# Performance work log

Hardware: AMD Instinct MI355X
Metric: run time of the kernel (lower is better)

Reference implementation:

```python
import jax, jax.numpy as jnp
import numpy as np

H = 8192  # hidden_size == input_size
NNZ = 1_000_000
B = 128
T = 64


def _spmm(rows, cols, values, x, out_dim):
    # y[r, :] += v * x[c, :] for each nnz (r, c, v); matches coalesced COO spmm
    gathered = values[:, None] * x[cols]          # [nnz, B]
    return jax.ops.segment_sum(gathered, rows, num_segments=out_dim)  # [out_dim, B]


def setup_inputs() -> dict:
    key = jax.random.key(0)
    ks = jax.random.split(key, 5)
    x = jax.random.normal(ks[0], (B, T, H), dtype=jnp.float32)
    ih_indices = jax.random.randint(ks[1], (2, NNZ), 0, H, dtype=jnp.int32)
    hh_indices = jax.random.randint(ks[2], (2, NNZ), 0, H, dtype=jnp.int32)
    # scale so tanh pre-activations stay in a reasonable range (~122 nnz/row)
    ih_values = jax.random.normal(ks[3], (NNZ,), dtype=jnp.float32) * 0.05
    hh_values = jax.random.normal(ks[4], (NNZ,), dtype=jnp.float32) * 0.05
    bias_ih = jnp.zeros((H, 1), dtype=jnp.float32)
    bias_hh = jnp.zeros((H, 1), dtype=jnp.float32)
    return {
        "x": x,
        "ih_indices": ih_indices,
        "ih_values": ih_values,
        "hh_indices": hh_indices,
        "hh_values": hh_values,
        "bias_ih": bias_ih,
        "bias_hh": bias_hh,
    }


def reference(x, ih_indices, ih_values, hh_indices, hh_values, bias_ih, bias_hh):
    # x: (batch, seq, features) -> (T, F, B) as in torch permute(1, 2, 0)
    xs = jnp.transpose(x, (1, 2, 0))  # [T, H, B]
    ih_r, ih_c = ih_indices[0], ih_indices[1]
    hh_r, hh_c = hh_indices[0], hh_indices[1]

    def step(h, x_t):
        pre = (_spmm(ih_r, ih_c, ih_values, x_t, H) + bias_ih
               + _spmm(hh_r, hh_c, hh_values, h, H) + bias_hh)
        h_new = jnp.tanh(pre)
        return h_new, h_new

    h0 = jnp.zeros((H, x.shape[0]), dtype=x.dtype)
    _, out = jax.lax.scan(step, h0, xs)  # out: [T, H, B]
    return jnp.transpose(out, (2, 0, 1))  # [B, T, H] (batch_first)
```

## Files before the change

kernel.cpp:

```cpp
#include <hip/hip_runtime.h>
#include <cstdint>
#include <cstddef>
#include <cstring>

#define H 8192
#define NNZ 1000000
#define B 128
#define T 64

typedef unsigned int u32;
typedef u32 u32x2 __attribute__((ext_vector_type(2)));

__device__ inline float bf_lo(u32 w) { return __uint_as_float(w << 16); }
__device__ inline float bf_hi(u32 w) { return __uint_as_float(w & 0xffff0000u); }
__device__ inline unsigned short f2bf(float f) {
    u32 v = __float_as_uint(f);
    v += 0x7fffu + ((v >> 16) & 1u);
    return (unsigned short)(v >> 16);
}
__device__ inline u32 pack_bf16(float a, float b) {
    return (u32)f2bf(a) | ((u32)f2bf(b) << 16);
}
__device__ inline float fast_tanh(float x) {
    float e = __expf(2.0f * x);
    return 1.0f - 2.0f / (e + 1.0f);
}

__device__ inline void spmm_row(const int* __restrict__ rp, const int2* __restrict__ pair,
                                const char* __restrict__ basep, int r, bool hi, u32 i8,
                                float& ax, float& ay, float& az, float& aw) {
    int s = rp[r], e = rp[r + 1];
    int j = s;
    for (; j + 16 <= e; j += 16) {
        int2 q[16];
        #pragma unroll
        for (int u = 0; u < 16; ++u) q[u] = pair[j + u];
        u32x2 g[8];
        #pragma unroll
        for (int u = 0; u < 8; ++u) {
            u32 c = (u32)(hi ? q[2 * u + 1].x : q[2 * u].x);
            g[u] = *(const u32x2*)(basep + ((c << 8) + i8));
        }
        #pragma unroll
        for (int u = 0; u < 8; ++u) {
            float v = __int_as_float(hi ? q[2 * u + 1].y : q[2 * u].y);
            ax = fmaf(v, bf_lo(g[u].x), ax);
            ay = fmaf(v, bf_hi(g[u].x), ay);
            az = fmaf(v, bf_lo(g[u].y), az);
            aw = fmaf(v, bf_hi(g[u].y), aw);
        }
    }
    for (; j + 2 <= e; j += 2) {
        int2 q0 = pair[j], q1 = pair[j + 1];
        u32 c = (u32)(hi ? q1.x : q0.x);
        u32x2 g = *(const u32x2*)(basep + ((c << 8) + i8));
        float v = __int_as_float(hi ? q1.y : q0.y);
        ax = fmaf(v, bf_lo(g.x), ax);
        ay = fmaf(v, bf_hi(g.x), ay);
        az = fmaf(v, bf_lo(g.y), az);
        aw = fmaf(v, bf_hi(g.y), aw);
    }
    if (j < e) {
        int2 q0 = pair[j];
        u32 c = (u32)q0.x;
        u32x2 g = *(const u32x2*)(basep + ((c << 8) + i8));
        float v = hi ? 0.0f : __int_as_float(q0.y);
        ax = fmaf(v, bf_lo(g.x), ax);
        ay = fmaf(v, bf_hi(g.x), ay);
        az = fmaf(v, bf_lo(g.y), az);
        aw = fmaf(v, bf_hi(g.y), aw);
    }
}

__global__ void hist2_kernel(const int* __restrict__ rows_a, const int* __restrict__ rows_b,
                             int* __restrict__ cnt_a, int* __restrict__ cnt_b) {
    int j = blockIdx.x * blockDim.x + threadIdx.x;
    if (j < NNZ) atomicAdd(&cnt_a[rows_a[j]], 1);
    else if (j < 2 * NNZ) atomicAdd(&cnt_b[rows_b[j - NNZ]], 1);
}

__global__ void scan_kernel(const int* __restrict__ cnt0, int* __restrict__ rp0, int* __restrict__ cur0,
                            const int* __restrict__ cnt1, int* __restrict__ rp1, int* __restrict__ cur1) {
    const int* cnt = (blockIdx.x == 0) ? cnt0 : cnt1;
    int* rp  = (blockIdx.x == 0) ? rp0 : rp1;
    int* cur = (blockIdx.x == 0) ? cur0 : cur1;
    __shared__ int buf[1024];
    __shared__ int carry;
    int tid = threadIdx.x;
    if (tid == 0) carry = 0;
    __syncthreads();
    for (int base = 0; base < H; base += 1024) {
        int v = cnt[base + tid];
        buf[tid] = v;
        __syncthreads();
        for (int off = 1; off < 1024; off <<= 1) {
            int t = (tid >= off) ? buf[tid - off] : 0;
            __syncthreads();
            buf[tid] += t;
            __syncthreads();
        }
        int incl = buf[tid];
        int excl = incl - v;
        int c = carry;
        rp[base + tid]  = c + excl;
        cur[base + tid] = c + excl;
        __syncthreads();
        if (tid == 1023) carry = c + incl;
        __syncthreads();
    }
    if (tid == 0) rp[H] = carry;
}

__global__ void scatter2_kernel(const int* __restrict__ ra, const int* __restrict__ ca,
                                const float* __restrict__ va, int* __restrict__ cur_a,
                                int2* __restrict__ pa,
                                const int* __restrict__ rb, const int* __restrict__ cb,
                                const float* __restrict__ vb, int* __restrict__ cur_b,
                                int2* __restrict__ pb) {
    int j = blockIdx.x * blockDim.x + threadIdx.x;
    if (j < NNZ) {
        int r = ra[j];
        int p = atomicAdd(&cur_a[r], 1);
        pa[p] = make_int2(ca[j], __float_as_int(va[j]));
    } else if (j < 2 * NNZ) {
        int jj = j - NNZ;
        int r = rb[jj];
        int p = atomicAdd(&cur_b[r], 1);
        pb[p] = make_int2(cb[jj], __float_as_int(vb[jj]));
    }
}

__global__ void transpose_bf16_kernel(const float* __restrict__ src, u32* __restrict__ dst) {
    __shared__ float tile[32][33];
    int c0 = blockIdx.x * 32;
    int r0 = blockIdx.y * 32;
    int x = threadIdx.x, y = threadIdx.y;
    #pragma unroll
    for (int i = y; i < 32; i += 8) {
        tile[i][x] = src[(size_t)(r0 + i) * (T * H) + (c0 + x)];
    }
    __syncthreads();
    int tid = y * 32 + x;
    #pragma unroll
    for (int idx = tid; idx < 32 * 16; idx += 256) {
        int row = idx >> 4, w = idx & 15;
        u32 word = pack_bf16(tile[2 * w][row], tile[2 * w + 1][row]);
        dst[(size_t)(c0 + row) * 64 + (r0 >> 1) + w] = word;
    }
}

__global__ void transpose_out_kernel(const u32* __restrict__ src, float* __restrict__ dst) {
    __shared__ u32 tile[32][33];
    int c0 = blockIdx.x * 32;
    int w0 = blockIdx.y * 32;
    int x = threadIdx.x, y = threadIdx.y;
    #pragma unroll
    for (int i = y; i < 32; i += 8) {
        tile[i][x] = src[(size_t)(c0 + i) * 64 + (w0 + x)];
    }
    __syncthreads();
    #pragma unroll
    for (int i = y; i < 64; i += 8) {
        int w = i >> 1;
        u32 word = tile[x][w];
        float val = (i & 1) ? bf_hi(word) : bf_lo(word);
        dst[(size_t)(2 * w0 + i) * (size_t)(T * H) + (c0 + x)] = val;
    }
}

__global__ void __launch_bounds__(256) ih_pre3_kernel(
    const int* __restrict__ rp, const int2* __restrict__ pair,
    const u32* __restrict__ xTb, u32* __restrict__ pre,
    const float* __restrict__ bias_ih, const float* __restrict__ bias_hh) {
    const int tid  = threadIdx.x;
    const int wav  = tid >> 6;
    const int lane = tid & 63;
    const bool hi  = lane >= 32;
    const int i    = lane & 31;
    const u32 i8   = (u32)i * 8u;
    const int w = __builtin_amdgcn_readfirstlane(((int)blockIdx.x << 2) + wav);
    const int t = w >> 13;
    const int r = w & (H - 1);
    const char* __restrict__ xtb = (const char*)(xTb + (size_t)t * H * 64);
    float ax = 0.f, ay = 0.f, az = 0.f, aw = 0.f;
    spmm_row(rp, pair, xtb, r, hi, i8, ax, ay, az, aw);
    float tx = ax + __shfl_xor(ax, 32, 64);
    float ty = ay + __shfl_xor(ay, 32, 64);
    float tz = az + __shfl_xor(az, 32, 64);
    float tw = aw + __shfl_xor(aw, 32, 64);
    if (lane < 32) {
        float bias = bias_ih[r] + bias_hh[r];
        u32x2 pw;
        pw.x = pack_bf16(tx + bias, ty + bias);
        pw.y = pack_bf16(tz + bias, tw + bias);
        __builtin_nontemporal_store(pw, (u32x2*)(pre + ((size_t)t * H + r) * 64) + i);
    }
}

__global__ void __launch_bounds__(256) fused_step_kernel(
    const int* __restrict__ rp_hh, const int2* __restrict__ pair_hh,
    const int* __restrict__ rp_ih, const int2* __restrict__ pair_ih,
    const u32* __restrict__ xTb, u32* __restrict__ pre,
    const u32* __restrict__ hprev, u32* __restrict__ hout,
    const u32* __restrict__ pre_t,
    const float* __restrict__ bias_ih, const float* __restrict__ bias_hh,
    int tpre) {
    const int tid  = threadIdx.x;
    const int wav  = tid >> 6;
    const int lane = tid & 63;
    const bool hi  = lane >= 32;
    const int i    = lane & 31;
    const u32 i8   = (u32)i * 8u;
    const int bid  = (int)blockIdx.x;
    if (bid < 2048) {
        const int r = __builtin_amdgcn_readfirstlane((bid << 2) + wav);
        u32x2 pw = __builtin_nontemporal_load((const u32x2*)pre_t + (size_t)r * 32 + i);
        float ax = 0.f, ay = 0.f, az = 0.f, aw = 0.f;
        if (hprev) {
            spmm_row(rp_hh, pair_hh, (const char*)hprev, r, hi, i8, ax, ay, az, aw);
            ax += __shfl_xor(ax, 32, 64);
            ay += __shfl_xor(ay, 32, 64);
            az += __shfl_xor(az, 32, 64);
            aw += __shfl_xor(aw, 32, 64);
        }
        if (lane < 32) {
            float h0 = fast_tanh(ax + bf_lo(pw.x));
            float h1 = fast_tanh(ay + bf_hi(pw.x));
            float h2v = fast_tanh(az + bf_lo(pw.y));
            float h3 = fast_tanh(aw + bf_hi(pw.y));
            u32x2 hw;
            hw.x = pack_bf16(h0, h1);
            hw.y = pack_bf16(h2v, h3);
            ((u32x2*)hout)[(size_t)r * 32 + i] = hw;
        }
    } else {
        const int r = __builtin_amdgcn_readfirstlane(((bid - 2048) << 2) + wav);
        const char* __restrict__ xtb = (const char*)(xTb + (size_t)tpre * H * 64);
        float ax = 0.f, ay = 0.f, az = 0.f, aw = 0.f;
        spmm_row(rp_ih, pair_ih, xtb, r, hi, i8, ax, ay, az, aw);
        float tx = ax + __shfl_xor(ax, 32, 64);
        float ty = ay + __shfl_xor(ay, 32, 64);
        float tz = az + __shfl_xor(az, 32, 64);
        float tw = aw + __shfl_xor(aw, 32, 64);
        if (lane < 32) {
            float bias = bias_ih[r] + bias_hh[r];
            u32x2 pw;
            pw.x = pack_bf16(tx + bias, ty + bias);
            pw.y = pack_bf16(tz + bias, tw + bias);
            __builtin_nontemporal_store(pw, (u32x2*)(pre + ((size_t)tpre * H + r) * 64) + i);
        }
    }
}

extern "C" void kernel_launch(void* const* d_in, const int* in_sizes, int n_in,
                              void* d_out, int out_size, void* d_ws, size_t ws_size,
                              hipStream_t stream) {
    const float* x        = (const float*)d_in[0];
    const int*   ih_idx   = (const int*)d_in[1];
    const float* ih_val   = (const float*)d_in[2];
    const int*   hh_idx   = (const int*)d_in[3];
    const float* hh_val   = (const float*)d_in[4];
    const float* bias_ih  = (const float*)d_in[5];
    const float* bias_hh  = (const float*)d_in[6];
    const int* ih_rows = ih_idx;
    const int* ih_cols = ih_idx + NNZ;
    const int* hh_rows = hh_idx;
    const int* hh_cols = hh_idx + NNZ;

    char* ws = (char*)d_ws;
    size_t off = 0;
    auto alloc = [&](size_t bytes) -> void* {
        void* p = ws + off;
        off += (bytes + 255) & ~(size_t)255;
        return p;
    };
    u32*   xTb     = (u32*)  alloc((size_t)T * H * 64 * 4);
    u32*   pre     = (u32*)  alloc((size_t)T * H * 64 * 4);
    u32*   outb    = (u32*)  alloc((size_t)T * H * 64 * 4);
    int2*  pair_ih = (int2*) alloc((size_t)NNZ * 8);
    int2*  pair_hh = (int2*) alloc((size_t)NNZ * 8);
    int*   rp_ih   = (int*)  alloc((size_t)(H + 1) * 4);
    int*   rp_hh   = (int*)  alloc((size_t)(H + 1) * 4);
    int*   cnt_ih  = (int*)  alloc((size_t)H * 4);
    int*   cnt_hh  = (int*)  alloc((size_t)H * 4);
    int*   cur_ih  = (int*)  alloc((size_t)H * 4);
    int*   cur_hh  = (int*)  alloc((size_t)H * 4);

    hipMemsetAsync(cnt_ih, 0, (size_t)H * 4, stream);
    hipMemsetAsync(cnt_hh, 0, (size_t)H * 4, stream);

    const int tb = 256;
    const int gb2 = (2 * NNZ + tb - 1) / tb;
    hist2_kernel<<<gb2, tb, 0, stream>>>(ih_rows, hh_rows, cnt_ih, cnt_hh);
    scan_kernel<<<2, 1024, 0, stream>>>(cnt_ih, rp_ih, cur_ih, cnt_hh, rp_hh, cur_hh);
    scatter2_kernel<<<gb2, tb, 0, stream>>>(ih_rows, ih_cols, ih_val, cur_ih, pair_ih,
                                            hh_rows, hh_cols, hh_val, cur_hh, pair_hh);

    dim3 tblk(32, 8);
    dim3 tgrid1((T * H) / 32, B / 32);
    transpose_bf16_kernel<<<tgrid1, tblk, 0, stream>>>(x, xTb);

    ih_pre3_kernel<<<(3 * H) / 4, 256, 0, stream>>>(rp_ih, pair_ih, xTb, pre, bias_ih, bias_hh);

    for (int t = 0; t < T; ++t) {
        int tpre = (t + 3 < T) ? (t + 3) : -1;
        int grid = (tpre >= 0) ? 4096 : 2048;
        fused_step_kernel<<<grid, 256, 0, stream>>>(
            rp_hh, pair_hh, rp_ih, pair_ih, xTb, pre,
            (t > 0) ? (outb + (size_t)(t - 1) * H * 64) : (const u32*)nullptr,
            outb + (size_t)t * H * 64,
            pre + (size_t)t * H * 64,
            bias_ih, bias_hh, tpre);
    }

    dim3 tgrid2((T * H) / 32, 2);
    transpose_out_kernel<<<tgrid2, tblk, 0, stream>>>(outb, (float*)d_out);
}
```

Measured before the change: 2.640 ms.

## Precompute all input projections upfront and balance recurrent rows by nnz

Input-to-hidden SpMM is no longer overlapped inside each step launch. All T timesteps are now computed in one big kernel before the recurrence, using one wave per row and an XCD-aware block-to-timestep mapping. A new single-block kernel counting-sorts hidden rows by nnz, and each step block pairs a long row with a short row so per-wave work evens out. This shrinks each recurrent step's grid and shortens its critical path, but loses the overlap of the ih work with the latency-bound steps and adds an indirection load per row.

```diff
diff --git a/kernel.cpp b/kernel.cpp
--- a/kernel.cpp
+++ b/kernel.cpp
@@ -130,6 +130,38 @@
     }
 }
 
+__global__ void __launch_bounds__(1024) sort_rows_kernel(const int* __restrict__ cnt,
+                                                         int* __restrict__ order) {
+    __shared__ int hist[1024];
+    __shared__ int cursor[1024];
+    int tid = threadIdx.x;
+    hist[tid] = 0;
+    __syncthreads();
+    for (int r = tid; r < H; r += 1024) {
+        int len = cnt[r]; if (len > 1023) len = 1023;
+        atomicAdd(&hist[len], 1);
+    }
+    __syncthreads();
+    int v = hist[tid];
+    cursor[tid] = v;
+    __syncthreads();
+    for (int off = 1; off < 1024; off <<= 1) {
+        int t = (tid >= off) ? cursor[tid - off] : 0;
+        __syncthreads();
+        cursor[tid] += t;
+        __syncthreads();
+    }
+    int excl = cursor[tid] - v;
+    __syncthreads();
+    cursor[tid] = excl;
+    __syncthreads();
+    for (int r = tid; r < H; r += 1024) {
+        int len = cnt[r]; if (len > 1023) len = 1023;
+        int p = atomicAdd(&cursor[len], 1);
+        order[H - 1 - p] = r;
+    }
+}
+
 __global__ void transpose_bf16_kernel(const float* __restrict__ src, u32* __restrict__ dst) {
     __shared__ float tile[32][33];
     int c0 = blockIdx.x * 32;
@@ -168,20 +200,20 @@
     }
 }
 
-__global__ void __launch_bounds__(256) ih_pre3_kernel(
+__global__ void __launch_bounds__(64) ih_pre_kernel(
     const int* __restrict__ rp, const int2* __restrict__ pair,
     const u32* __restrict__ xTb, u32* __restrict__ pre,
     const float* __restrict__ bias_ih, const float* __restrict__ bias_hh) {
-    const int tid  = threadIdx.x;
-    const int wav  = tid >> 6;
-    const int lane = tid & 63;
-    const bool hi  = lane >= 32;
-    const int i    = lane & 31;
-    const u32 i8   = (u32)i * 8u;
-    const int w = __builtin_amdgcn_readfirstlane(((int)blockIdx.x << 2) + wav);
-    const int t = w >> 13;
-    const int r = w & (H - 1);
+    int bid = blockIdx.x;
+    int xcd = bid & 7;
+    int i0  = bid >> 3;
+    int t   = (xcd << 3) + (i0 >> 13);
+    int r   = i0 & (H - 1);
+    int lane = threadIdx.x;
+    bool hi = lane >= 32;
+    int i = lane & 31;
     const char* __restrict__ xtb = (const char*)(xTb + (size_t)t * H * 64);
+    const u32 i8 = (u32)i * 8u;
     float ax = 0.f, ay = 0.f, az = 0.f, aw = 0.f;
     spmm_row(rp, pair, xtb, r, hi, i8, ax, ay, az, aw);
     float tx = ax + __shfl_xor(ax, 32, 64);
@@ -197,27 +229,25 @@
     }
 }
 
-__global__ void __launch_bounds__(256) fused_step_kernel(
-    const int* __restrict__ rp_hh, const int2* __restrict__ pair_hh,
-    const int* __restrict__ rp_ih, const int2* __restrict__ pair_ih,
-    const u32* __restrict__ xTb, u32* __restrict__ pre,
+__global__ void __launch_bounds__(256) step_kernel(
+    const int* __restrict__ rp, const int2* __restrict__ pair,
+    const int* __restrict__ order,
     const u32* __restrict__ hprev, u32* __restrict__ hout,
-    const u32* __restrict__ pre_t,
-    const float* __restrict__ bias_ih, const float* __restrict__ bias_hh,
-    int tpre) {
+    const u32* __restrict__ pre_t) {
     const int tid  = threadIdx.x;
     const int wav  = tid >> 6;
     const int lane = tid & 63;
     const bool hi  = lane >= 32;
     const int i    = lane & 31;
     const u32 i8   = (u32)i * 8u;
-    const int bid  = (int)blockIdx.x;
-    if (bid < 2048) {
-        const int r = __builtin_amdgcn_readfirstlane((bid << 2) + wav);
+    const int w = ((int)blockIdx.x << 2) + wav;
+    #pragma unroll
+    for (int half = 0; half < 2; ++half) {
+        const int r = __builtin_amdgcn_readfirstlane(order[half ? (H - 1 - w) : w]);
         u32x2 pw = __builtin_nontemporal_load((const u32x2*)pre_t + (size_t)r * 32 + i);
         float ax = 0.f, ay = 0.f, az = 0.f, aw = 0.f;
         if (hprev) {
-            spmm_row(rp_hh, pair_hh, (const char*)hprev, r, hi, i8, ax, ay, az, aw);
+            spmm_row(rp, pair, (const char*)hprev, r, hi, i8, ax, ay, az, aw);
             ax += __shfl_xor(ax, 32, 64);
             ay += __shfl_xor(ay, 32, 64);
             az += __shfl_xor(az, 32, 64);
@@ -232,22 +262,6 @@
             hw.x = pack_bf16(h0, h1);
             hw.y = pack_bf16(h2v, h3);
             ((u32x2*)hout)[(size_t)r * 32 + i] = hw;
-        }
-    } else {
-        const int r = __builtin_amdgcn_readfirstlane(((bid - 2048) << 2) + wav);
-        const char* __restrict__ xtb = (const char*)(xTb + (size_t)tpre * H * 64);
-        float ax = 0.f, ay = 0.f, az = 0.f, aw = 0.f;
-        spmm_row(rp_ih, pair_ih, xtb, r, hi, i8, ax, ay, az, aw);
-        float tx = ax + __shfl_xor(ax, 32, 64);
-        float ty = ay + __shfl_xor(ay, 32, 64);
-        float tz = az + __shfl_xor(az, 32, 64);
-        float tw = aw + __shfl_xor(aw, 32, 64);
-        if (lane < 32) {
-            float bias = bias_ih[r] + bias_hh[r];
-            u32x2 pw;
-            pw.x = pack_bf16(tx + bias, ty + bias);
-            pw.y = pack_bf16(tz + bias, tw + bias);
-            __builtin_nontemporal_store(pw, (u32x2*)(pre + ((size_t)tpre * H + r) * 64) + i);
         }
     }
 }
@@ -285,6 +299,7 @@
     int*   cnt_hh  = (int*)  alloc((size_t)H * 4);
     int*   cur_ih  = (int*)  alloc((size_t)H * 4);
     int*   cur_hh  = (int*)  alloc((size_t)H * 4);
+    int*   order   = (int*)  alloc((size_t)H * 4);
 
     hipMemsetAsync(cnt_ih, 0, (size_t)H * 4, stream);
     hipMemsetAsync(cnt_hh, 0, (size_t)H * 4, stream);
@@ -295,22 +310,21 @@
     scan_kernel<<<2, 1024, 0, stream>>>(cnt_ih, rp_ih, cur_ih, cnt_hh, rp_hh, cur_hh);
     scatter2_kernel<<<gb2, tb, 0, stream>>>(ih_rows, ih_cols, ih_val, cur_ih, pair_ih,
                                             hh_rows, hh_cols, hh_val, cur_hh, pair_hh);
+    sort_rows_kernel<<<1, 1024, 0, stream>>>(cnt_hh, order);
 
     dim3 tblk(32, 8);
     dim3 tgrid1((T * H) / 32, B / 32);
     transpose_bf16_kernel<<<tgrid1, tblk, 0, stream>>>(x, xTb);
 
-    ih_pre3_kernel<<<(3 * H) / 4, 256, 0, stream>>>(rp_ih, pair_ih, xTb, pre, bias_ih, bias_hh);
-
-    for (int t = 0; t < T; ++t) {
-        int tpre = (t + 3 < T) ? (t + 3) : -1;
-        int grid = (tpre >= 0) ? 4096 : 2048;
-        fused_step_kernel<<<grid, 256, 0, stream>>>(
-            rp_hh, pair_hh, rp_ih, pair_ih, xTb, pre,
-            (t > 0) ? (outb + (size_t)(t - 1) * H * 64) : (const u32*)nullptr,
-            outb + (size_t)t * H * 64,
-            pre + (size_t)t * H * 64,
-            bias_ih, bias_hh, tpre);
+    ih_pre_kernel<<<T * H, 64, 0, stream>>>(rp_ih, pair_ih, xTb, pre, bias_ih, bias_hh);
+
+    step_kernel<<<H / 8, 256, 0, stream>>>(rp_hh, pair_hh, order, (const u32*)nullptr,
+                                           outb, pre);
+    for (int t = 1; t < T; ++t) {
+        step_kernel<<<H / 8, 256, 0, stream>>>(rp_hh, pair_hh, order,
+                                               outb + (size_t)(t - 1) * H * 64,
+                                               outb + (size_t)t * H * 64,
+                                               pre + (size_t)t * H * 64);
     }
 
     dim3 tgrid2((T * H) / 32, 2);
```

Measured after the change: 2.693 ms. About the same (+2.0%).
